# Optimization experiments

Hardware: AMD Instinct MI355X
Metric: run time of the kernel (lower is better)

Reference implementation:

```python
import jax, jax.numpy as jnp
import numpy as np

NEG_SLOPE = 0.2  # LeakyReLU(0.2) on the final Dense


def setup_inputs() -> dict:
    key = jax.random.key(0)
    k1, k2, k3, k4 = jax.random.split(key, 4)
    B, D = 256, 65536          # batch, input voxel dim
    N, G = 41, 2048            # n_groups, group size (overlapping allowed)
    O, E = 256, 512            # per-group output dim, embed_dim
    x = jax.random.normal(k1, (B, D), dtype=jnp.float32)
    group_idx = jax.random.randint(k2, (N, G), 0, D, dtype=jnp.int32)
    # He-normal-ish init for the per-group Dense weights
    W = jax.random.normal(k3, (N, G, O), dtype=jnp.float32) * np.float32(np.sqrt(2.0 / G))
    b = jnp.zeros((N, O), dtype=jnp.float32)
    W3 = jax.random.normal(k4, (N * O, E), dtype=jnp.float32) * np.float32(np.sqrt(2.0 / (N * O)))
    b3 = jnp.zeros((E,), dtype=jnp.float32)
    return {"x": x, "group_idx": group_idx, "W": W, "b": b, "W3": W3, "b3": b3}


def reference(x, group_idx, W, b, W3, b3):
    B = x.shape[0]
    # per-group gather: (B, N, G)
    g = x[:, group_idx]
    # N parallel Dense layers as one grouped GEMM: (B, N, O)
    h = jnp.einsum('bng,ngo->bno', g, W) + b
    # concat along feature axis -> (B, N*O); dropout is identity at inference
    h = h.reshape(B, -1)
    # final Dense + LeakyReLU(0.2)
    out = h @ W3 + b3
    return jnp.where(out >= 0, out, NEG_SLOPE * out)
```

## Files before the change

### kernel.cpp

```cpp
#include <hip/hip_runtime.h>
#include <hip/hip_bf16.h>

#define NB 256
#define DD 65536
#define NN 41
#define GG 2048
#define OO 256
#define NO 10496
#define EE 512
#define NEG_SLOPE 0.2f

typedef __attribute__((ext_vector_type(8))) short bf16x8;
typedef __attribute__((ext_vector_type(4))) float f32x4;
typedef unsigned int u32;

__device__ __forceinline__ void gl_lds16(const __hip_bfloat16* gsrc, __hip_bfloat16* lds) {
    __builtin_amdgcn_global_load_lds((const __attribute__((address_space(1))) u32*)gsrc,
                                     (__attribute__((address_space(3))) u32*)lds, 16, 0, 0);
}

__device__ __forceinline__ u32 pack_bf2(float lo, float hi) {
    u32 a = (u32)__bfloat16_as_ushort(__float2bfloat16(lo));
    u32 b = (u32)__bfloat16_as_ushort(__float2bfloat16(hi));
    return a | (b << 16);
}

__global__ __launch_bounds__(256) void transpose_w3_k(const float* __restrict__ W3,
                                                      __hip_bfloat16* __restrict__ W3t) {
    __shared__ u32 tb[64 * 128];
    int rem = blockIdx.x;
    int kc0 = (rem >> 3) * 256;
    int o0 = (rem & 7) * 64;
    int t = threadIdx.x;
    int p = t & 127;
    int oh = (t >> 7) * 32;
    const float* r0 = W3 + (size_t)(kc0 + 2 * p) * EE + o0 + oh;
    const float* r1 = r0 + EE;
#pragma unroll
    for (int c = 0; c < 8; ++c) {
        float4 a = *(const float4*)&r0[c * 4];
        float4 b = *(const float4*)&r1[c * 4];
        tb[(oh + c * 4 + 0) * 128 + p] = pack_bf2(a.x, b.x);
        tb[(oh + c * 4 + 1) * 128 + p] = pack_bf2(a.y, b.y);
        tb[(oh + c * 4 + 2) * 128 + p] = pack_bf2(a.z, b.z);
        tb[(oh + c * 4 + 3) * 128 + p] = pack_bf2(a.w, b.w);
    }
    __syncthreads();
    int w = t >> 6, l = t & 63;
    int lr = l >> 5;
    int ls = l & 31;
#pragma unroll
    for (int j = 0; j < 8; ++j) {
        int o = j * 8 + w * 2 + lr;
        uint4 v = *(const uint4*)&tb[o * 128 + ls * 4];
        *(uint4*)&W3t[(size_t)(o0 + o) * NO + kc0 + ls * 8] = v;
    }
}

__global__ __launch_bounds__(1024) void prep_k(const float* __restrict__ x,
                                               const int* __restrict__ idx,
                                               const float* __restrict__ W3,
                                               __hip_bfloat16* __restrict__ g,
                                               __hip_bfloat16* __restrict__ W3t) {
    extern __shared__ __hip_bfloat16 xr[];
    int t = threadIdx.x;
    if (blockIdx.x < NB) {
        int b = blockIdx.x;
        const float4* xv = (const float4*)(x + (size_t)b * DD);
#pragma unroll
        for (int i = 0; i < 16; ++i) {
            float4 v = xv[t + 1024 * i];
            short4 p;
            p.x = (short)__bfloat16_as_ushort(__float2bfloat16(v.x));
            p.y = (short)__bfloat16_as_ushort(__float2bfloat16(v.y));
            p.z = (short)__bfloat16_as_ushort(__float2bfloat16(v.z));
            p.w = (short)__bfloat16_as_ushort(__float2bfloat16(v.w));
            *(short4*)&xr[(t + 1024 * i) * 4] = p;
        }
        __syncthreads();
        const int4* idx4 = (const int4*)idx;
        for (int u = t; u < NN * GG / 4; u += 1024) {
            int4 ii = idx4[u];
            int n = u >> 9;
            int k = (u & 511) * 4;
            ushort4 o;
            o.x = __bfloat16_as_ushort(xr[ii.x]);
            o.y = __bfloat16_as_ushort(xr[ii.y]);
            o.z = __bfloat16_as_ushort(xr[ii.z]);
            o.w = __bfloat16_as_ushort(xr[ii.w]);
            *(ushort4*)&g[((size_t)n * NB + b) * GG + k] = o;
        }
    } else {
        int c = blockIdx.x - NB;
        int kc0 = (c >> 3) * 256;
        int o0 = (c & 7) * 64;
        u32* tb = (u32*)xr;
        int p = t & 127;
        int oh = (t >> 7) * 8;
        const float* r0 = W3 + (size_t)(kc0 + 2 * p) * EE + o0 + oh;
        const float* r1 = r0 + EE;
#pragma unroll
        for (int cc = 0; cc < 2; ++cc) {
            float4 a = *(const float4*)&r0[cc * 4];
            float4 b = *(const float4*)&r1[cc * 4];
            tb[(oh + cc * 4 + 0) * 128 + p] = pack_bf2(a.x, b.x);
            tb[(oh + cc * 4 + 1) * 128 + p] = pack_bf2(a.y, b.y);
            tb[(oh + cc * 4 + 2) * 128 + p] = pack_bf2(a.z, b.z);
            tb[(oh + cc * 4 + 3) * 128 + p] = pack_bf2(a.w, b.w);
        }
        __syncthreads();
        int o = t >> 4;
        int ls = t & 15;
        uint4 v0 = *(const uint4*)&tb[o * 128 + ls * 4];
        uint4 v1 = *(const uint4*)&tb[o * 128 + (ls + 16) * 4];
        __hip_bfloat16* drow = &W3t[(size_t)(o0 + o) * NO + kc0];
        *(uint4*)&drow[ls * 8] = v0;
        *(uint4*)&drow[(ls + 16) * 8] = v1;
    }
}

__global__ __launch_bounds__(512) void gather_half_k(const float* __restrict__ x,
                                                     const int* __restrict__ idx,
                                                     __hip_bfloat16* __restrict__ g) {
    __shared__ __align__(16) __hip_bfloat16 xr[32768];
    int b = blockIdx.x >> 1;
    int h = blockIdx.x & 1;
    int t = threadIdx.x;
    const float4* xv = (const float4*)(x + (size_t)b * DD + h * 32768);
#pragma unroll
    for (int i = 0; i < 16; ++i) {
        float4 v = xv[t + 512 * i];
        short4 p;
        p.x = (short)__bfloat16_as_ushort(__float2bfloat16(v.x));
        p.y = (short)__bfloat16_as_ushort(__float2bfloat16(v.y));
        p.z = (short)__bfloat16_as_ushort(__float2bfloat16(v.z));
        p.w = (short)__bfloat16_as_ushort(__float2bfloat16(v.w));
        *(short4*)&xr[(t + 512 * i) * 4] = p;
    }
    __syncthreads();
    const int4* idx4 = (const int4*)idx;
    for (int u = t; u < NN * GG / 4; u += 512) {
        int4 ii = idx4[u];
        int n = u >> 9;
        int k = (u & 511) * 4;
        __hip_bfloat16* dst = &g[((size_t)n * NB + b) * GG + k];
        if ((ii.x >> 15) == h) dst[0] = xr[ii.x & 32767];
        if ((ii.y >> 15) == h) dst[1] = xr[ii.y & 32767];
        if ((ii.z >> 15) == h) dst[2] = xr[ii.z & 32767];
        if ((ii.w >> 15) == h) dst[3] = xr[ii.w & 32767];
    }
}

__global__ __launch_bounds__(512) void gemm1_k(const __hip_bfloat16* __restrict__ g,
                                               const float* __restrict__ W,
                                               __hip_bfloat16* __restrict__ part1) {
    int bid0 = blockIdx.x;
    int bid = (bid0 & 7) * 41 + (bid0 >> 3);
    int s = bid & 3;
    int o0 = ((bid >> 2) & 1) * 128;
    int n = bid >> 3;
    const __hip_bfloat16* srcA = g + (size_t)n * NB * GG + s * 512;
    const float* srcB = W + ((size_t)n * GG + s * 512) * OO + o0;
    __shared__ __align__(16) __hip_bfloat16 lA[2][256 * 32];
    __shared__ __align__(16) u32 lB[2][128 * 16];
    int t = threadIdx.x;
    int lane = t & 63, w = t >> 6;
    int mw = (w >> 1) * 64, ow = (w & 1) * 64;
    int lrow = lane & 15, quad = lane >> 4;
    int r0 = t >> 2, q0 = (t & 3) * 8;
    int bp = (t >> 4) & 15;
    int boq8 = t & 15;
    int hi = w >> 2;
    int cb = boq8 * 8 + hi * 4;
    int pw = bp ^ ((boq8 & 3) << 2);
    const __hip_bfloat16* aR = srcA + (size_t)r0 * GG + q0;
    const __hip_bfloat16* aS = srcA + (size_t)(r0 + 128) * GG + q0;
    const float* wb0 = srcB + (size_t)(2 * bp) * OO + cb;
    f32x4 acc[4][4] = {};

    uint4 axl, axh; float4 bxa, bxb;
    uint4 ayl, ayh; float4 bya, byb;

#define LOADX(kk) { axl = *(const uint4*)&aR[kk]; axh = *(const uint4*)&aS[kk]; \
                    const float* wn_ = wb0 + (size_t)(kk) * OO; \
                    bxa = *(const float4*)&wn_[0]; bxb = *(const float4*)&wn_[OO]; }
#define LOADY(kk) { ayl = *(const uint4*)&aR[kk]; ayh = *(const uint4*)&aS[kk]; \
                    const float* wn_ = wb0 + (size_t)(kk) * OO; \
                    bya = *(const float4*)&wn_[0]; byb = *(const float4*)&wn_[OO]; }
#define STOREX(buf) { *(uint4*)&lA[buf][t * 8] = axl; *(uint4*)&lA[buf][(t + 512) * 8] = axh; \
                      u32* d_ = &lB[buf][0]; \
                      d_[(cb + 0) * 16 + pw] = pack_bf2(bxa.x, bxb.x); \
                      d_[(cb + 1) * 16 + pw] = pack_bf2(bxa.y, bxb.y); \
                      d_[(cb + 2) * 16 + pw] = pack_bf2(bxa.z, bxb.z); \
                      d_[(cb + 3) * 16 + pw] = pack_bf2(bxa.w, bxb.w); }
#define STOREY(buf) { *(uint4*)&lA[buf][t * 8] = ayl; *(uint4*)&lA[buf][(t + 512) * 8] = ayh; \
                      u32* d_ = &lB[buf][0]; \
                      d_[(cb + 0) * 16 + pw] = pack_bf2(bya.x, byb.x); \
                      d_[(cb + 1) * 16 + pw] = pack_bf2(bya.y, byb.y); \
                      d_[(cb + 2) * 16 + pw] = pack_bf2(bya.z, byb.z); \
                      d_[(cb + 3) * 16 + pw] = pack_bf2(bya.w, byb.w); }
#define MMA(buf) { bf16x8 af[4]; \
    _Pragma("unroll") for (int fm = 0; fm < 4; ++fm) \
        af[fm] = *(const bf16x8*)&lA[buf][(mw + fm * 16 + lrow) * 32 + quad * 8]; \
    const u32* lbu = &lB[buf][0]; \
    _Pragma("unroll") for (int fn = 0; fn < 4; ++fn) { \
        int orow = ow + fn * 16 + lrow; \
        int fsw = ((orow >> 3) & 3) << 2; \
        bf16x8 bfr = *(const bf16x8*)&lbu[orow * 16 + (quad * 4 ^ fsw)]; \
        _Pragma("unroll") for (int fm = 0; fm < 4; ++fm) \
            acc[fm][fn] = __builtin_amdgcn_mfma_f32_16x16x32_bf16(af[fm], bfr, acc[fm][fn], 0, 0, 0); } }

    LOADX(0);
    LOADY(32);
    STOREX(0);
    __syncthreads();
#pragma unroll 1
    for (int j = 0; j < 8; ++j) {
        int itE = 2 * j;
        if (itE + 2 < 16) LOADX((itE + 2) * 32);
        MMA(0);
        STOREY(1);
        __syncthreads();
        if (itE + 3 < 16) LOADY((itE + 3) * 32);
        MMA(1);
        if (itE + 2 < 16) STOREX(0);
        __syncthreads();
    }
#undef LOADX
#undef LOADY
#undef STOREX
#undef STOREY
#undef MMA
#pragma unroll
    for (int fm = 0; fm < 4; ++fm) {
#pragma unroll
        for (int fn = 0; fn < 4; ++fn) {
            int col = o0 + ow + fn * 16 + lrow;
#pragma unroll
            for (int r = 0; r < 4; ++r) {
                int row = mw + fm * 16 + quad * 4 + r;
                part1[((size_t)s * NB + row) * NO + n * OO + col] = __float2bfloat16(acc[fm][fn][r]);
            }
        }
    }
}

__global__ __launch_bounds__(256) void combine1_k(const __hip_bfloat16* __restrict__ part1,
                                                  const float* __restrict__ bias,
                                                  __hip_bfloat16* __restrict__ h) {
    int j4 = blockIdx.x * 256 + threadIdx.x;
    int jj = j4 % (NO / 4);
    float4 a = ((const float4*)bias)[jj];
#pragma unroll
    for (int s = 0; s < 4; ++s) {
        ushort4 p = *(const ushort4*)&part1[(size_t)s * NB * NO + (size_t)j4 * 4];
        a.x += __bfloat162float(__ushort_as_bfloat16(p.x));
        a.y += __bfloat162float(__ushort_as_bfloat16(p.y));
        a.z += __bfloat162float(__ushort_as_bfloat16(p.z));
        a.w += __bfloat162float(__ushort_as_bfloat16(p.w));
    }
    ushort4 o;
    o.x = __bfloat16_as_ushort(__float2bfloat16(a.x));
    o.y = __bfloat16_as_ushort(__float2bfloat16(a.y));
    o.z = __bfloat16_as_ushort(__float2bfloat16(a.z));
    o.w = __bfloat16_as_ushort(__float2bfloat16(a.w));
    *(ushort4*)&h[(size_t)j4 * 4] = o;
}

__global__ __launch_bounds__(256) void gemm2_k(const __hip_bfloat16* __restrict__ h,
                                               const __hip_bfloat16* __restrict__ W3t,
                                               float* __restrict__ part) {
    int bid0 = blockIdx.x;
    int bid = (bid0 & 7) * 82 + (bid0 >> 3);
    int e0 = (bid & 7) * 64;
    int m0 = ((bid >> 3) & 1) * 128;
    int s = bid >> 4;
    const __hip_bfloat16* srcA = h + (size_t)m0 * NO + s * 256;
    const __hip_bfloat16* srcB = W3t + (size_t)e0 * NO + s * 256;
    __shared__ __align__(16) __hip_bfloat16 lA[2][128 * 32];
    __shared__ __align__(16) __hip_bfloat16 lB[2][64 * 32];
    int t = threadIdx.x;
    int lane = t & 63, w = t >> 6;
    int mw = (w >> 1) * 64, ew = (w & 1) * 32;
    int lrow = lane & 15, quad = lane >> 4;
    int rA = t >> 2, qA = (t & 3) * 8;
    int rB = t >> 2, qB = (t & 3) * 8;
    f32x4 acc[4][2] = {};

    gl_lds16(srcA + (size_t)rA * NO + qA, &lA[0][t * 8]);
    gl_lds16(srcA + (size_t)(rA + 64) * NO + qA, &lA[0][(t + 256) * 8]);
    gl_lds16(srcB + (size_t)(rB & 63) * NO + qB, &lB[0][t * 8]);
    __syncthreads();
#pragma unroll 1
    for (int it = 0; it < 8; ++it) {
        int cur = it & 1;
        if (it + 1 < 8) {
            int k1 = (it + 1) * 32;
            gl_lds16(srcA + (size_t)rA * NO + k1 + qA, &lA[1 - cur][t * 8]);
            gl_lds16(srcA + (size_t)(rA + 64) * NO + k1 + qA, &lA[1 - cur][(t + 256) * 8]);
            gl_lds16(srcB + (size_t)(rB & 63) * NO + k1 + qB, &lB[1 - cur][t * 8]);
        }
        bf16x8 af[4];
#pragma unroll
        for (int fm = 0; fm < 4; ++fm)
            af[fm] = *(const bf16x8*)&lA[cur][(mw + fm * 16 + lrow) * 32 + quad * 8];
#pragma unroll
        for (int fn = 0; fn < 2; ++fn) {
            bf16x8 bfr = *(const bf16x8*)&lB[cur][(ew + fn * 16 + lrow) * 32 + quad * 8];
#pragma unroll
            for (int fm = 0; fm < 4; ++fm)
                acc[fm][fn] = __builtin_amdgcn_mfma_f32_16x16x32_bf16(af[fm], bfr, acc[fm][fn], 0, 0, 0);
        }
        __syncthreads();
    }
#pragma unroll
    for (int fm = 0; fm < 4; ++fm) {
#pragma unroll
        for (int fn = 0; fn < 2; ++fn) {
            int e = e0 + ew + fn * 16 + lrow;
#pragma unroll
            for (int r = 0; r < 4; ++r) {
                int row = m0 + mw + fm * 16 + quad * 4 + r;
                part[((size_t)s * NB + row) * EE + e] = acc[fm][fn][r];
            }
        }
    }
}

__global__ __launch_bounds__(128) void reduce_k(const float* __restrict__ part,
                                                const float* __restrict__ b3,
                                                float* __restrict__ out) {
    int j = blockIdx.x * 128 + threadIdx.x;
    float4 a = make_float4(0.f, 0.f, 0.f, 0.f);
    for (int s = 0; s < NN; ++s) {
        float4 v = ((const float4*)part)[(size_t)s * (NB * EE / 4) + j];
        a.x += v.x; a.y += v.y; a.z += v.z; a.w += v.w;
    }
    float4 bv = ((const float4*)b3)[j & 127];
    a.x += bv.x; a.y += bv.y; a.z += bv.z; a.w += bv.w;
    a.x = a.x >= 0.f ? a.x : NEG_SLOPE * a.x;
    a.y = a.y >= 0.f ? a.y : NEG_SLOPE * a.y;
    a.z = a.z >= 0.f ? a.z : NEG_SLOPE * a.z;
    a.w = a.w >= 0.f ? a.w : NEG_SLOPE * a.w;
    ((float4*)out)[j] = a;
}

extern "C" void kernel_launch(void* const* d_in, const int* in_sizes, int n_in,
                              void* d_out, int out_size, void* d_ws, size_t ws_size,
                              hipStream_t stream) {
    const float* x = (const float*)d_in[0];
    const int* idx = (const int*)d_in[1];
    const float* W = (const float*)d_in[2];
    const float* bias = (const float*)d_in[3];
    const float* W3 = (const float*)d_in[4];
    const float* b3 = (const float*)d_in[5];
    float* out = (float*)d_out;

    char* ws = (char*)d_ws;
    const size_t g_off = 0;
    const size_t g_sz = (size_t)NN * NB * GG * 2;
    const size_t wt_off = g_off + g_sz;
    const size_t wt_sz = (size_t)NN * GG * OO * 2;
    const size_t w3t_off = wt_off + wt_sz;
    const size_t w3t_sz = (size_t)NO * EE * 2;
    const size_t h_off = w3t_off + w3t_sz;
    const size_t h_sz = (size_t)NB * NO * 2;
    const size_t p_off = h_off + h_sz;

    __hip_bfloat16* g = (__hip_bfloat16*)(ws + g_off);
    __hip_bfloat16* W3t = (__hip_bfloat16*)(ws + w3t_off);
    __hip_bfloat16* h = (__hip_bfloat16*)(ws + h_off);
    __hip_bfloat16* part1 = (__hip_bfloat16*)(ws + wt_off);
    float* part = (float*)(ws + p_off);

    hipError_t aerr = hipFuncSetAttribute(reinterpret_cast<const void*>(prep_k),
                                          hipFuncAttributeMaxDynamicSharedMemorySize, 131072);
    if (aerr == hipSuccess) {
        prep_k<<<dim3(NB + NN * 8), 1024, 131072, stream>>>(x, idx, W3, g, W3t);
    } else {
        transpose_w3_k<<<dim3(NN * 8), 256, 0, stream>>>(W3, W3t);
        gather_half_k<<<dim3(512), 512, 0, stream>>>(x, idx, g);
    }
    gemm1_k<<<dim3(328), 512, 0, stream>>>(g, W, part1);
    combine1_k<<<dim3(NB * NO / 4 / 256), 256, 0, stream>>>(part1, bias, h);
    gemm2_k<<<dim3(656), 256, 0, stream>>>(h, W3t, part);
    reduce_k<<<dim3(256), 128, 0, stream>>>(part, b3, out);
}
```

Baseline: 263.4 us.

## Retile both GEMMs and batch gather index loads for more memory parallelism

The gather loop in prep_k now loads four index vectors per iteration before issuing the LDS reads and global stores, which raises memory-level parallelism. gemm1 is split along the batch dimension into 128-row tiles with 256-thread blocks, doubling the grid to 656 blocks. Each thread now converts 8 W columns instead of 4, so W is read and converted to bf16 twice, once per batch half. gemm2 moves to 128x128 tiles with a register-staged double buffer in place of direct global-to-LDS loads, halving its grid. The goal is better occupancy and load balance in gemm1 and more reuse per block in gemm2, at the cost of more register pressure and extra W traffic.

```diff
diff --git a/kernel.cpp b/kernel.cpp
--- a/kernel.cpp
+++ b/kernel.cpp
@@ -79,16 +79,35 @@
         }
         __syncthreads();
         const int4* idx4 = (const int4*)idx;
-        for (int u = t; u < NN * GG / 4; u += 1024) {
+#pragma unroll 1
+        for (int i = 0; i < 5; ++i) {
+            int u0 = t + i * 4096;
+            int4 ia = idx4[u0];
+            int4 ib = idx4[u0 + 1024];
+            int4 ic = idx4[u0 + 2048];
+            int4 id = idx4[u0 + 3072];
+            ushort4 oa, ob, oc, od;
+            oa.x = __bfloat16_as_ushort(xr[ia.x]); oa.y = __bfloat16_as_ushort(xr[ia.y]);
+            oa.z = __bfloat16_as_ushort(xr[ia.z]); oa.w = __bfloat16_as_ushort(xr[ia.w]);
+            ob.x = __bfloat16_as_ushort(xr[ib.x]); ob.y = __bfloat16_as_ushort(xr[ib.y]);
+            ob.z = __bfloat16_as_ushort(xr[ib.z]); ob.w = __bfloat16_as_ushort(xr[ib.w]);
+            oc.x = __bfloat16_as_ushort(xr[ic.x]); oc.y = __bfloat16_as_ushort(xr[ic.y]);
+            oc.z = __bfloat16_as_ushort(xr[ic.z]); oc.w = __bfloat16_as_ushort(xr[ic.w]);
+            od.x = __bfloat16_as_ushort(xr[id.x]); od.y = __bfloat16_as_ushort(xr[id.y]);
+            od.z = __bfloat16_as_ushort(xr[id.z]); od.w = __bfloat16_as_ushort(xr[id.w]);
+            int u;
+            u = u0;        *(ushort4*)&g[((size_t)(u >> 9) * NB + b) * GG + (u & 511) * 4] = oa;
+            u = u0 + 1024; *(ushort4*)&g[((size_t)(u >> 9) * NB + b) * GG + (u & 511) * 4] = ob;
+            u = u0 + 2048; *(ushort4*)&g[((size_t)(u >> 9) * NB + b) * GG + (u & 511) * 4] = oc;
+            u = u0 + 3072; *(ushort4*)&g[((size_t)(u >> 9) * NB + b) * GG + (u & 511) * 4] = od;
+        }
+        if (t < 512) {
+            int u = t + 20480;
             int4 ii = idx4[u];
-            int n = u >> 9;
-            int k = (u & 511) * 4;
             ushort4 o;
-            o.x = __bfloat16_as_ushort(xr[ii.x]);
-            o.y = __bfloat16_as_ushort(xr[ii.y]);
-            o.z = __bfloat16_as_ushort(xr[ii.z]);
-            o.w = __bfloat16_as_ushort(xr[ii.w]);
-            *(ushort4*)&g[((size_t)n * NB + b) * GG + k] = o;
+            o.x = __bfloat16_as_ushort(xr[ii.x]); o.y = __bfloat16_as_ushort(xr[ii.y]);
+            o.z = __bfloat16_as_ushort(xr[ii.z]); o.w = __bfloat16_as_ushort(xr[ii.w]);
+            *(ushort4*)&g[((size_t)(u >> 9) * NB + b) * GG + (u & 511) * 4] = o;
         }
     } else {
         int c = blockIdx.x - NB;
@@ -151,54 +170,64 @@
     }
 }
 
-__global__ __launch_bounds__(512) void gemm1_k(const __hip_bfloat16* __restrict__ g,
+__global__ __launch_bounds__(256) void gemm1_k(const __hip_bfloat16* __restrict__ g,
                                                const float* __restrict__ W,
                                                __hip_bfloat16* __restrict__ part1) {
     int bid0 = blockIdx.x;
-    int bid = (bid0 & 7) * 41 + (bid0 >> 3);
+    int bid = (bid0 & 7) * 82 + (bid0 >> 3);
     int s = bid & 3;
     int o0 = ((bid >> 2) & 1) * 128;
-    int n = bid >> 3;
-    const __hip_bfloat16* srcA = g + (size_t)n * NB * GG + s * 512;
+    int m0 = ((bid >> 3) & 1) * 128;
+    int n = bid >> 4;
+    const __hip_bfloat16* srcA = g + ((size_t)n * NB + m0) * GG + s * 512;
     const float* srcB = W + ((size_t)n * GG + s * 512) * OO + o0;
-    __shared__ __align__(16) __hip_bfloat16 lA[2][256 * 32];
+    __shared__ __align__(16) __hip_bfloat16 lA[2][128 * 32];
     __shared__ __align__(16) u32 lB[2][128 * 16];
     int t = threadIdx.x;
     int lane = t & 63, w = t >> 6;
     int mw = (w >> 1) * 64, ow = (w & 1) * 64;
     int lrow = lane & 15, quad = lane >> 4;
     int r0 = t >> 2, q0 = (t & 3) * 8;
-    int bp = (t >> 4) & 15;
-    int boq8 = t & 15;
-    int hi = w >> 2;
-    int cb = boq8 * 8 + hi * 4;
-    int pw = bp ^ ((boq8 & 3) << 2);
+    int bp = t >> 4;
+    int boq = t & 15;
+    int pw = bp ^ ((boq & 3) << 2);
+    int cb = boq * 8;
     const __hip_bfloat16* aR = srcA + (size_t)r0 * GG + q0;
-    const __hip_bfloat16* aS = srcA + (size_t)(r0 + 128) * GG + q0;
+    const __hip_bfloat16* aS = srcA + (size_t)(r0 + 64) * GG + q0;
     const float* wb0 = srcB + (size_t)(2 * bp) * OO + cb;
     f32x4 acc[4][4] = {};
 
-    uint4 axl, axh; float4 bxa, bxb;
-    uint4 ayl, ayh; float4 bya, byb;
+    uint4 axl, axh; float4 bxa, bxb, bxc, bxd;
+    uint4 ayl, ayh; float4 bya, byb, byc, byd;
 
 #define LOADX(kk) { axl = *(const uint4*)&aR[kk]; axh = *(const uint4*)&aS[kk]; \
                     const float* wn_ = wb0 + (size_t)(kk) * OO; \
-                    bxa = *(const float4*)&wn_[0]; bxb = *(const float4*)&wn_[OO]; }
+                    bxa = *(const float4*)&wn_[0];  bxc = *(const float4*)&wn_[4]; \
+                    bxb = *(const float4*)&wn_[OO]; bxd = *(const float4*)&wn_[OO + 4]; }
 #define LOADY(kk) { ayl = *(const uint4*)&aR[kk]; ayh = *(const uint4*)&aS[kk]; \
                     const float* wn_ = wb0 + (size_t)(kk) * OO; \
-                    bya = *(const float4*)&wn_[0]; byb = *(const float4*)&wn_[OO]; }
-#define STOREX(buf) { *(uint4*)&lA[buf][t * 8] = axl; *(uint4*)&lA[buf][(t + 512) * 8] = axh; \
+                    bya = *(const float4*)&wn_[0];  byc = *(const float4*)&wn_[4]; \
+                    byb = *(const float4*)&wn_[OO]; byd = *(const float4*)&wn_[OO + 4]; }
+#define STOREX(buf) { *(uint4*)&lA[buf][t * 8] = axl; *(uint4*)&lA[buf][(t + 256) * 8] = axh; \
                       u32* d_ = &lB[buf][0]; \
                       d_[(cb + 0) * 16 + pw] = pack_bf2(bxa.x, bxb.x); \
                       d_[(cb + 1) * 16 + pw] = pack_bf2(bxa.y, bxb.y); \
                       d_[(cb + 2) * 16 + pw] = pack_bf2(bxa.z, bxb.z); \
-                      d_[(cb + 3) * 16 + pw] = pack_bf2(bxa.w, bxb.w); }
-#define STOREY(buf) { *(uint4*)&lA[buf][t * 8] = ayl; *(uint4*)&lA[buf][(t + 512) * 8] = ayh; \
+                      d_[(cb + 3) * 16 + pw] = pack_bf2(bxa.w, bxb.w); \
+                      d_[(cb + 4) * 16 + pw] = pack_bf2(bxc.x, bxd.x); \
+                      d_[(cb + 5) * 16 + pw] = pack_bf2(bxc.y, bxd.y); \
+                      d_[(cb + 6) * 16 + pw] = pack_bf2(bxc.z, bxd.z); \
+                      d_[(cb + 7) * 16 + pw] = pack_bf2(bxc.w, bxd.w); }
+#define STOREY(buf) { *(uint4*)&lA[buf][t * 8] = ayl; *(uint4*)&lA[buf][(t + 256) * 8] = ayh; \
                       u32* d_ = &lB[buf][0]; \
                       d_[(cb + 0) * 16 + pw] = pack_bf2(bya.x, byb.x); \
                       d_[(cb + 1) * 16 + pw] = pack_bf2(bya.y, byb.y); \
                       d_[(cb + 2) * 16 + pw] = pack_bf2(bya.z, byb.z); \
-                      d_[(cb + 3) * 16 + pw] = pack_bf2(bya.w, byb.w); }
+                      d_[(cb + 3) * 16 + pw] = pack_bf2(bya.w, byb.w); \
+                      d_[(cb + 4) * 16 + pw] = pack_bf2(byc.x, byd.x); \
+                      d_[(cb + 5) * 16 + pw] = pack_bf2(byc.y, byd.y); \
+                      d_[(cb + 6) * 16 + pw] = pack_bf2(byc.z, byd.z); \
+                      d_[(cb + 7) * 16 + pw] = pack_bf2(byc.w, byd.w); }
 #define MMA(buf) { bf16x8 af[4]; \
     _Pragma("unroll") for (int fm = 0; fm < 4; ++fm) \
         af[fm] = *(const bf16x8*)&lA[buf][(mw + fm * 16 + lrow) * 32 + quad * 8]; \
@@ -238,7 +267,7 @@
             int col = o0 + ow + fn * 16 + lrow;
 #pragma unroll
             for (int r = 0; r < 4; ++r) {
-                int row = mw + fm * 16 + quad * 4 + r;
+                int row = m0 + mw + fm * 16 + quad * 4 + r;
                 part1[((size_t)s * NB + row) * NO + n * OO + col] = __float2bfloat16(acc[fm][fn][r]);
             }
         }
@@ -271,52 +300,69 @@
                                                const __hip_bfloat16* __restrict__ W3t,
                                                float* __restrict__ part) {
     int bid0 = blockIdx.x;
-    int bid = (bid0 & 7) * 82 + (bid0 >> 3);
-    int e0 = (bid & 7) * 64;
-    int m0 = ((bid >> 3) & 1) * 128;
-    int s = bid >> 4;
+    int bid = (bid0 & 7) * 41 + (bid0 >> 3);
+    int e0 = (bid & 3) * 128;
+    int m0 = ((bid >> 2) & 1) * 128;
+    int s = bid >> 3;
     const __hip_bfloat16* srcA = h + (size_t)m0 * NO + s * 256;
     const __hip_bfloat16* srcB = W3t + (size_t)e0 * NO + s * 256;
     __shared__ __align__(16) __hip_bfloat16 lA[2][128 * 32];
-    __shared__ __align__(16) __hip_bfloat16 lB[2][64 * 32];
+    __shared__ __align__(16) __hip_bfloat16 lB[2][128 * 32];
     int t = threadIdx.x;
     int lane = t & 63, w = t >> 6;
-    int mw = (w >> 1) * 64, ew = (w & 1) * 32;
+    int mw = (w >> 1) * 64, ew = (w & 1) * 64;
     int lrow = lane & 15, quad = lane >> 4;
-    int rA = t >> 2, qA = (t & 3) * 8;
-    int rB = t >> 2, qB = (t & 3) * 8;
-    f32x4 acc[4][2] = {};
-
-    gl_lds16(srcA + (size_t)rA * NO + qA, &lA[0][t * 8]);
-    gl_lds16(srcA + (size_t)(rA + 64) * NO + qA, &lA[0][(t + 256) * 8]);
-    gl_lds16(srcB + (size_t)(rB & 63) * NO + qB, &lB[0][t * 8]);
+    int r0 = t >> 2, q0 = (t & 3) * 8;
+    const __hip_bfloat16* aR = srcA + (size_t)r0 * NO + q0;
+    const __hip_bfloat16* aS = srcA + (size_t)(r0 + 64) * NO + q0;
+    const __hip_bfloat16* bR = srcB + (size_t)r0 * NO + q0;
+    const __hip_bfloat16* bS = srcB + (size_t)(r0 + 64) * NO + q0;
+    f32x4 acc[4][4] = {};
+
+    uint4 axl, axh, bxl, bxh;
+    uint4 ayl, ayh, byl, byh;
+
+#define LOADX2(kk) { axl = *(const uint4*)&aR[kk]; axh = *(const uint4*)&aS[kk]; \
+                     bxl = *(const uint4*)&bR[kk]; bxh = *(const uint4*)&bS[kk]; }
+#define LOADY2(kk) { ayl = *(const uint4*)&aR[kk]; ayh = *(const uint4*)&aS[kk]; \
+                     byl = *(const uint4*)&bR[kk]; byh = *(const uint4*)&bS[kk]; }
+#define STOREX2(buf) { *(uint4*)&lA[buf][t * 8] = axl; *(uint4*)&lA[buf][(t + 256) * 8] = axh; \
+                       *(uint4*)&lB[buf][t * 8] = bxl; *(uint4*)&lB[buf][(t + 256) * 8] = bxh; }
+#define STOREY2(buf) { *(uint4*)&lA[buf][t * 8] = ayl; *(uint4*)&lA[buf][(t + 256) * 8] = ayh; \
+                       *(uint4*)&lB[buf][t * 8] = byl; *(uint4*)&lB[buf][(t + 256) * 8] = byh; }
+#define MMA2(buf) { bf16x8 af[4]; \
+    _Pragma("unroll") for (int fm = 0; fm < 4; ++fm) \
+        af[fm] = *(const bf16x8*)&lA[buf][(mw + fm * 16 + lrow) * 32 + quad * 8]; \
+    _Pragma("unroll") for (int fn = 0; fn < 4; ++fn) { \
+        bf16x8 bfr = *(const bf16x8*)&lB[buf][(ew + fn * 16 + lrow) * 32 + quad * 8]; \
+        _Pragma("unroll") for (int fm = 0; fm < 4; ++fm) \
+            acc[fm][fn] = __builtin_amdgcn_mfma_f32_16x16x32_bf16(af[fm], bfr, acc[fm][fn], 0, 0, 0); } }
+
+    LOADX2(0);
+    LOADY2(32);
+    STOREX2(0);
     __syncthreads();
 #pragma unroll 1
-    for (int it = 0; it < 8; ++it) {
-        int cur = it & 1;
-        if (it + 1 < 8) {
-            int k1 = (it + 1) * 32;
-            gl_lds16(srcA + (size_t)rA * NO + k1 + qA, &lA[1 - cur][t * 8]);
-            gl_lds16(srcA + (size_t)(rA + 64) * NO + k1 + qA, &lA[1 - cur][(t + 256) * 8]);
-            gl_lds16(srcB + (size_t)(rB & 63) * NO + k1 + qB, &lB[1 - cur][t * 8]);
-        }
-        bf16x8 af[4];
-#pragma unroll
-        for (int fm = 0; fm < 4; ++fm)
-            af[fm] = *(const bf16x8*)&lA[cur][(mw + fm * 16 + lrow) * 32 + quad * 8];
-#pragma unroll
-        for (int fn = 0; fn < 2; ++fn) {
-            bf16x8 bfr = *(const bf16x8*)&lB[cur][(ew + fn * 16 + lrow) * 32 + quad * 8];
-#pragma unroll
-            for (int fm = 0; fm < 4; ++fm)
-                acc[fm][fn] = __builtin_amdgcn_mfma_f32_16x16x32_bf16(af[fm], bfr, acc[fm][fn], 0, 0, 0);
-        }
-        __syncthreads();
-    }
+    for (int j = 0; j < 4; ++j) {
+        int itE = 2 * j;
+        if (itE + 2 < 8) LOADX2((itE + 2) * 32);
+        MMA2(0);
+        STOREY2(1);
+        __syncthreads();
+        if (itE + 3 < 8) LOADY2((itE + 3) * 32);
+        MMA2(1);
+        if (itE + 2 < 8) STOREX2(0);
+        __syncthreads();
+    }
+#undef LOADX2
+#undef LOADY2
+#undef STOREX2
+#undef STOREY2
+#undef MMA2
 #pragma unroll
     for (int fm = 0; fm < 4; ++fm) {
 #pragma unroll
-        for (int fn = 0; fn < 2; ++fn) {
+        for (int fn = 0; fn < 4; ++fn) {
             int e = e0 + ew + fn * 16 + lrow;
 #pragma unroll
             for (int r = 0; r < 4; ++r) {
@@ -381,8 +427,8 @@
         transpose_w3_k<<<dim3(NN * 8), 256, 0, stream>>>(W3, W3t);
         gather_half_k<<<dim3(512), 512, 0, stream>>>(x, idx, g);
     }
-    gemm1_k<<<dim3(328), 512, 0, stream>>>(g, W, part1);
+    gemm1_k<<<dim3(656), 256, 0, stream>>>(g, W, part1);
     combine1_k<<<dim3(NB * NO / 4 / 256), 256, 0, stream>>>(part1, bias, h);
-    gemm2_k<<<dim3(656), 256, 0, stream>>>(h, W3t, part);
+    gemm2_k<<<dim3(328), 256, 0, stream>>>(h, W3t, part);
     reduce_k<<<dim3(256), 128, 0, stream>>>(part, b3, out);
 }
```

New measurement: 258.1 us. -2.0%, faster.
